# Kernel tuning notes

Hardware: AMD Instinct MI355X
Metric: run time of the kernel (lower is better)

Reference implementation:

```python
import jax, jax.numpy as jnp
import numpy as np
from jax import lax

ALPHA = 2.0       # spikingjelly ATan surrogate default alpha
NUM_HEADS = 8
V_TH = 1.0

@jax.custom_vjp
def spike(x):
    return (x >= 0.0).astype(x.dtype)

def _spike_fwd(x):
    return spike(x), x

def _spike_bwd(x, g):
    # ATan surrogate: alpha/2 / (1 + (pi/2 * alpha * x)^2)
    return (g * (ALPHA / 2.0) / (1.0 + (jnp.pi / 2.0 * ALPHA * x) ** 2),)

spike.defvjp(_spike_fwd, _spike_bwd)

def lif(x, w):
    # ParametricLIFNode, step_mode='m', decay_input=True, hard reset to 0,
    # detach_reset=True. x: [T, ...]; w: learned scalar, decay = sigmoid(w).
    decay = jax.nn.sigmoid(w)
    def step(v, xt):
        v = v + (xt - v) * decay
        s = spike(v - V_TH)
        v = v * (1.0 - lax.stop_gradient(s))  # detach_reset hard reset
        return v, s
    _, s = lax.scan(step, jnp.zeros_like(x[0]), x)
    return s

def layernorm(x, g, b, eps=1e-5):
    m = x.mean(-1, keepdims=True)
    var = ((x - m) ** 2).mean(-1, keepdims=True)
    return (x - m) / jnp.sqrt(var + eps) * g + b

def setup_inputs() -> dict:
    key = jax.random.key(0)
    ks = jax.random.split(key, 16)
    T, B, C, H, W = 4, 16, 512, 16, 16
    hidden = 4 * C
    s = 0.02
    inp = {
        'x': jax.random.normal(ks[0], (T, B, C, H, W), jnp.float32),
        'conv_w': jax.random.normal(ks[1], (C, 1, 3, 3), jnp.float32) * s,
        'conv_b': jnp.zeros((C,), jnp.float32),
        'ln1_g': jnp.ones((C,), jnp.float32),
        'ln1_b': jnp.zeros((C,), jnp.float32),
        'qkv_w': jax.random.normal(ks[2], (3 * C, C), jnp.float32) * s,
        'proj_w': jax.random.normal(ks[3], (C, C), jnp.float32) * s,
        'proj_b': jnp.zeros((C,), jnp.float32),
        'ln2_g': jnp.ones((C,), jnp.float32),
        'ln2_b': jnp.zeros((C,), jnp.float32),
        'fc1_w': jax.random.normal(ks[4], (hidden, C), jnp.float32) * s,
        'fc1_b': jnp.zeros((hidden,), jnp.float32),
        'fc2_w': jax.random.normal(ks[5], (C, hidden), jnp.float32) * s,
        'fc2_b': jnp.zeros((C,), jnp.float32),
        'lif_w': jnp.zeros((8,), jnp.float32),  # init_tau=2 -> w=0
    }
    return inp

def reference(x, conv_w, conv_b, ln1_g, ln1_b, qkv_w, proj_w, proj_b,
              ln2_g, ln2_b, fc1_w, fc1_b, fc2_w, fc2_b, lif_w):
    T, B, C, H, W = x.shape
    N = H * W
    nH = NUM_HEADS
    d = C // nH
    scale = d ** -0.5

    # conv positional embedding on spikes, residual
    s = lif(x, lif_w[0])
    sf = s.reshape(T * B, C, H, W)
    pos = lax.conv_general_dilated(
        sf, conv_w, (1, 1), 'SAME', feature_group_count=C,
        dimension_numbers=('NCHW', 'OIHW', 'NCHW'))
    pos = pos + conv_b[None, :, None, None]
    x = x + pos.reshape(T, B, C, H, W)

    # tokens: [T, B, N, C]
    xt = x.reshape(T, B, C, N).transpose(0, 1, 3, 2)

    # spiking linear attention
    h = lif(layernorm(xt, ln1_g, ln1_b), lif_w[1])
    qkv = h @ qkv_w.T                              # [T,B,N,3C]
    qkv = qkv.reshape(T, B, N, 3, nH, d).transpose(3, 0, 1, 4, 2, 5)  # [3,T,B,h,N,d]
    q = lif(qkv[0], lif_w[2])
    k = lif(qkv[1], lif_w[3])
    v = lif(qkv[2], lif_w[4])
    kv = jnp.einsum('tbhnd,tbhne->tbhde', k, v)    # [T,B,h,d,d]
    a = jnp.einsum('tbhnd,tbhde->tbhne', q, kv) * scale
    a = a.transpose(0, 1, 3, 2, 4).reshape(T, B, N, C)
    a = lif(a, lif_w[5])
    a = a @ proj_w.T + proj_b
    xt = xt + a

    # spiking MLP
    h = lif(layernorm(xt, ln2_g, ln2_b), lif_w[6])
    h = h @ fc1_w.T + fc1_b
    h = lif(h, lif_w[7])
    h = h @ fc2_w.T + fc2_b
    xt = xt + h

    return xt.transpose(0, 1, 3, 2).reshape(T, B, C, H, W)
```

## Files before the change

### kernel.cpp

```cpp
#include <hip/hip_runtime.h>

typedef unsigned long long u64;
typedef unsigned int u32;
typedef float  floatx4 __attribute__((ext_vector_type(4)));
typedef short  short8  __attribute__((ext_vector_type(8)));

#define T_ 4

static __device__ __forceinline__ float b2f(unsigned short u){
  union { unsigned int i; float f; } x; x.i = ((unsigned int)u) << 16; return x.f;
}
static __device__ __forceinline__ unsigned short f2b(float f){
  unsigned int u = __float_as_uint(f);
  unsigned int r = (u + 0x7FFFu + ((u >> 16) & 1u)) >> 16;
  return (unsigned short)r;
}
static __device__ __forceinline__ float sigmoidf_(float x){ return 1.f / (1.f + expf(-x)); }

static __device__ __forceinline__ void gll16(const void* g, void* l){
  __builtin_amdgcn_global_load_lds(
      (const __attribute__((address_space(1))) void*)g,
      (__attribute__((address_space(3))) void*)l, 16, 0, 0);
}

__global__ __launch_bounds__(256) void wsplit_kernel(const float* __restrict__ qkvw,
    const float* __restrict__ projw, const float* __restrict__ fc1w,
    const float* __restrict__ fc2w, unsigned short* __restrict__ hi,
    unsigned short* __restrict__ lo){
  int i = blockIdx.x * 256 + threadIdx.x;
  const float* src; int off;
  if (i < 786432)      { src = qkvw; off = i; }
  else if (i < 1048576){ src = projw; off = i - 786432; }
  else if (i < 2097152){ src = fc1w;  off = i - 1048576; }
  else                 { src = fc2w;  off = i - 2097152; }
  float f = src[off];
  unsigned short h = f2b(f);
  float r = f - b2f(h);
  hi[i] = h; lo[i] = f2b(r);
}

__global__ __launch_bounds__(256) void conv_lif_kernel(const float* __restrict__ x,
    const float* __restrict__ cw, const float* __restrict__ cb,
    const float* __restrict__ lifw, float* __restrict__ xt){
  __shared__ __align__(16) float xs[16 * 260];
  __shared__ u64 sbits[16][5];
  int bb = blockIdx.x & 15, cg = blockIdx.x >> 4;
  int c0 = cg * 16;
  int tid = threadIdx.x;
  int lane = tid & 63, w = tid >> 6;
  int cl = tid & 15;
  float D = sigmoidf_(lifw[0]);
  float cwv[9];
  #pragma unroll
  for (int j = 0; j < 9; ++j) cwv[j] = cw[(c0 + cl) * 9 + j];
  float cbv = cb[c0 + cl];
  float v[16];
  #pragma unroll
  for (int k = 0; k < 16; ++k) v[k] = 0.f;

  for (int t = 0; t < T_; ++t){
    #pragma unroll
    for (int j = 0; j < 4; ++j){
      int kk = __builtin_amdgcn_readfirstlane(w + 4 * j);
      const float* grow = x + (((size_t)t * 16 + bb) * 512 + c0 + kk) * 256 + lane * 4;
      gll16(grow, &xs[kk * 260]);
    }
    __syncthreads();
    #pragma unroll
    for (int k = 0; k < 16; ++k){
      float xv = xs[k * 260 + tid];
      v[k] = v[k] + (xv - v[k]) * D;
      bool sp = v[k] >= 1.f;
      u64 bal = __ballot(sp);
      if (lane == 0) sbits[k][w] = bal;
      v[k] = sp ? 0.f : v[k];
    }
    __syncthreads();
    u64 sw0 = sbits[cl][0], sw1 = sbits[cl][1], sw2 = sbits[cl][2], sw3 = sbits[cl][3];
    #pragma unroll
    for (int i = 0; i < 16; ++i){
      int n = (tid >> 4) + 16 * i;
      int hh = n >> 4, ww = n & 15;
      float acc = cbv;
      #pragma unroll
      for (int dy = -1; dy <= 1; ++dy){
        int yy = hh + dy; if ((unsigned)yy >= 16u) continue;
        #pragma unroll
        for (int dx = -1; dx <= 1; ++dx){
          int xx = ww + dx; if ((unsigned)xx >= 16u) continue;
          int p = yy * 16 + xx;
          u64 word = (p < 64) ? sw0 : (p < 128) ? sw1 : (p < 192) ? sw2 : sw3;
          if ((word >> (p & 63)) & 1ull) acc += cwv[(dy + 1) * 3 + (dx + 1)];
        }
      }
      float xv = xs[cl * 260 + n];
      xt[(((size_t)t * 16 + bb) * 256 + n) * 512 + c0 + cl] = xv + acc;
    }
    __syncthreads();
  }
}

__global__ __launch_bounds__(256) void ln_lif_kernel(const float* __restrict__ xt,
    const float* __restrict__ g, const float* __restrict__ be,
    const float* __restrict__ lifw, int lidx, u64* __restrict__ obits){
  int bn = blockIdx.x; int tid = threadIdx.x;
  int lane = tid & 63, wid = tid >> 6;
  int c0 = tid, c1 = tid + 256;
  __shared__ float ps[8];
  float D = sigmoidf_(lifw[lidx]);
  float g0 = g[c0], g1 = g[c1];
  float b0 = be[c0], b1 = be[c1];
  float v0 = 0.f, v1 = 0.f;
  for (int t = 0; t < T_; ++t){
    size_t base = ((size_t)t * 4096 + bn) * 512;
    float x0 = xt[base + c0], x1 = xt[base + c1];
    float s = x0 + x1, q = x0 * x0 + x1 * x1;
    #pragma unroll
    for (int m = 32; m > 0; m >>= 1){
      s += __shfl_xor(s, m, 64);
      q += __shfl_xor(q, m, 64);
    }
    if (lane == 0){ ps[wid * 2] = s; ps[wid * 2 + 1] = q; }
    __syncthreads();
    float S = ps[0] + ps[2] + ps[4] + ps[6];
    float Q = ps[1] + ps[3] + ps[5] + ps[7];
    __syncthreads();
    float mean = S * (1.f / 512.f);
    float var = Q * (1.f / 512.f) - mean * mean;
    float inv = 1.f / sqrtf(var + 1e-5f);
    float y0 = (x0 - mean) * inv * g0 + b0;
    float y1 = (x1 - mean) * inv * g1 + b1;
    v0 = v0 + (y0 - v0) * D; bool s0 = v0 >= 1.f;
    v1 = v1 + (y1 - v1) * D; bool s1 = v1 >= 1.f;
    u64 bal0 = __ballot(s0);
    u64 bal1 = __ballot(s1);
    if (lane == 0){
      size_t rb = ((size_t)t * 4096 + bn) * 8;
      obits[rb + wid] = bal0;
      obits[rb + 4 + wid] = bal1;
    }
    v0 = s0 ? 0.f : v0; v1 = s1 ? 0.f : v1;
  }
}

__global__ __launch_bounds__(256) void lif_bits_kernel(const float* __restrict__ in,
    u64* __restrict__ bits, const float* __restrict__ lifw, int lidx){
  int tid = blockIdx.x * 256 + threadIdx.x;
  int j = tid & 511; int bn = tid >> 9;
  float D = sigmoidf_(lifw[lidx]);
  float v = 0.f;
  #pragma unroll
  for (int t = 0; t < T_; ++t){
    int m = t * 4096 + bn;
    float xv = in[(size_t)m * 512 + j];
    v = v + (xv - v) * D;
    bool sp = v >= 1.f;
    u64 bal = __ballot(sp);
    if ((threadIdx.x & 63) == 0) bits[(size_t)m * 8 + (j >> 6)] = bal;
    v = sp ? 0.f : v;
  }
}

__global__ __launch_bounds__(256) void gemm_fused(
    const u64* __restrict__ Abits, int ars,
    const unsigned short* __restrict__ Whi, const unsigned short* __restrict__ Wlo, int ldw,
    const float* __restrict__ bias,
    float* __restrict__ xtio, float* __restrict__ outF,
    u64* __restrict__ outBits,
    int K, int mode, const float* __restrict__ lifw, int lidx){
  extern __shared__ __align__(16) char smemraw[];
  unsigned short* Bh = (unsigned short*)smemraw;
  unsigned short* Bl = (unsigned short*)(smemraw + 16384);
  u32* Alds = (u32*)(smemraw + 32768);
  u64* tab  = (u64*)(smemraw + 40960);
  int bn0 = blockIdx.x * 32;
  int n0  = blockIdx.y * 128;
  int tid = threadIdx.x, lane = tid & 63, wid = tid >> 6;
  int wn = wid * 32;
  int lm = lane & 15, quad = lane >> 4;
  int qs = quad * 8;
  int swz = ((lane & 3) ^ ((lane >> 3) & 3)) * 8;
  int rW = wn + (lane >> 2);
  const unsigned short* pH0 = Whi + (size_t)(n0 + rW) * ldw + swz;
  const unsigned short* pH1 = pH0 + (size_t)16 * ldw;
  const unsigned short* pL0 = Wlo + (size_t)(n0 + rW) * ldw + swz;
  const unsigned short* pL1 = pL0 + (size_t)16 * ldw;
  int b0 = __builtin_amdgcn_readfirstlane(wid << 10);
  int sx = (quad ^ ((lm >> 1) & 3)) << 3;

  auto stageA = [&](int w0){
    #pragma unroll
    for (int i = 0; i < 4; ++i){
      int idx = tid + i * 256;
      int r = idx & 127, w64 = idx >> 7;
      size_t g = (size_t)((r >> 5) * 4096 + bn0 + (r & 31));
      u64 vb = Abits[g * ars + w0 + w64];
      Alds[(2 * w64) * 128 + r]     = (u32)vb;
      Alds[(2 * w64 + 1) * 128 + r] = (u32)(vb >> 32);
    }
  };
  auto stageB = [&](int buf, int kb){
    int bo = (buf << 12) + b0;
    gll16(pH0 + kb, Bh + bo);
    gll16(pH1 + kb, Bh + bo + 512);
    gll16(pL0 + kb, Bl + bo);
    gll16(pL1 + kb, Bl + bo + 512);
  };

  if (tid < 16){
    u64 e = 0;
    #pragma unroll
    for (int j = 0; j < 4; ++j) if ((tid >> j) & 1) e |= 0x3F80ull << (16 * j);
    tab[tid] = e;
  }
  stageA(0);
  stageB(0, 0);
  stageB(1, 32);
  __syncthreads();

  floatx4 acc[8][2];
  #pragma unroll
  for (int i = 0; i < 8; ++i)
    #pragma unroll
    for (int j = 0; j < 2; ++j){ acc[i][j][0]=0.f; acc[i][j][1]=0.f; acc[i][j][2]=0.f; acc[i][j][3]=0.f; }

  int cur = 0;
  for (int kb = 0; kb < K; kb += 32){
    if (kb && (kb & 511) == 0){
      __syncthreads();
      stageA(kb >> 6);
      __syncthreads();
    }
    if (kb + 32 < K) asm volatile("s_waitcnt vmcnt(4)" ::: "memory");
    else             asm volatile("s_waitcnt vmcnt(0)" ::: "memory");
    __builtin_amdgcn_sched_barrier(0);
    int bo = cur << 12;
    int wl = (kb >> 5) & 15;
    short8 bh[2], bl[2];
    #pragma unroll
    for (int in = 0; in < 2; ++in){
      bh[in] = *(const short8*)(&Bh[bo + (wn + in * 16 + lm) * 32 + sx]);
      bl[in] = *(const short8*)(&Bl[bo + (wn + in * 16 + lm) * 32 + sx]);
    }
    __builtin_amdgcn_s_setprio(1);
    #pragma unroll
    for (int im = 0; im < 8; ++im){
      u32 wv = Alds[wl * 128 + im * 16 + lm];
      u32 by = wv >> qs;
      union { u64 d[2]; short8 s; } c;
      c.d[0] = tab[by & 15u];
      c.d[1] = tab[(by >> 4) & 15u];
      acc[im][0] = __builtin_amdgcn_mfma_f32_16x16x32_bf16(c.s, bh[0], acc[im][0], 0, 0, 0);
      acc[im][1] = __builtin_amdgcn_mfma_f32_16x16x32_bf16(c.s, bh[1], acc[im][1], 0, 0, 0);
      acc[im][0] = __builtin_amdgcn_mfma_f32_16x16x32_bf16(c.s, bl[0], acc[im][0], 0, 0, 0);
      acc[im][1] = __builtin_amdgcn_mfma_f32_16x16x32_bf16(c.s, bl[1], acc[im][1], 0, 0, 0);
    }
    __builtin_amdgcn_s_setprio(0);
    __builtin_amdgcn_sched_barrier(0);
    if (kb + 64 < K) stageB(cur, kb + 64);
    cur ^= 1;
  }

  if (mode == 0 || mode == 3){
    #pragma unroll
    for (int im = 0; im < 8; ++im){
      int row0 = im * 16 + quad * 4;
      #pragma unroll
      for (int in = 0; in < 2; ++in){
        int col = n0 + wn + in * 16 + lm;
        float bv = bias ? bias[col] : 0.f;
        #pragma unroll
        for (int r = 0; r < 4; ++r){
          int row = row0 + r;
          int t = row >> 5; int bq = bn0 + (row & 31);
          size_t gg = (size_t)t * 4096 + bq;
          float vv = acc[im][in][r] + bv + xtio[gg * 512 + col];
          if (mode == 0){
            xtio[gg * 512 + col] = vv;
          } else {
            outF[(((size_t)t * 16 + (bq >> 8)) * 512 + col) * 256 + (bq & 255)] = vv;
          }
        }
      }
    }
    return;
  }

  __syncthreads();
  u32* bits32 = (u32*)(smemraw + 32768);
  u64* ob; int obrs, obwb;
  if (mode == 1){ ob = outBits + (size_t)(n0 >> 9) * 131072; obrs = 8; obwb = (n0 & 511) >> 6; }
  else          { ob = outBits; obrs = 32; obwb = n0 >> 6; }
  float D = sigmoidf_(lifw[mode == 1 ? (2 + (n0 >> 9)) : lidx]);
  float bv0 = bias ? bias[n0 + wn + lm] : 0.f;
  float bv1 = bias ? bias[n0 + wn + 16 + lm] : 0.f;
  #pragma unroll
  for (int r = 0; r < 4; ++r){
    float vA0 = 0.f, vA1 = 0.f, vB0 = 0.f, vB1 = 0.f;
    #pragma unroll
    for (int t = 0; t < 4; ++t){
      float pA0 = acc[2*t][0][r] + bv0;   vA0 += (pA0 - vA0) * D; bool sA0 = vA0 >= 1.f; vA0 = sA0 ? 0.f : vA0;
      float pA1 = acc[2*t][1][r] + bv1;   vA1 += (pA1 - vA1) * D; bool sA1 = vA1 >= 1.f; vA1 = sA1 ? 0.f : vA1;
      float pB0 = acc[2*t+1][0][r] + bv0; vB0 += (pB0 - vB0) * D; bool sB0 = vB0 >= 1.f; vB0 = sB0 ? 0.f : vB0;
      float pB1 = acc[2*t+1][1][r] + bv1; vB1 += (pB1 - vB1) * D; bool sB1 = vB1 >= 1.f; vB1 = sB1 ? 0.f : vB1;
      u64 balA0 = __ballot(sA0), balA1 = __ballot(sA1);
      u64 balB0 = __ballot(sB0), balB1 = __ballot(sB1);
      if (lane < 4){
        int q = lane;
        u32 wA = (u32)((balA0 >> (16*q)) & 0xFFFFull) | ((u32)((balA1 >> (16*q)) & 0xFFFFull) << 16);
        u32 wB = (u32)((balB0 >> (16*q)) & 0xFFFFull) | ((u32)((balB1 >> (16*q)) & 0xFFFFull) << 16);
        bits32[(t * 32 + q * 4 + r) * 4 + wid]      = wA;
        bits32[(t * 32 + 16 + q * 4 + r) * 4 + wid] = wB;
      }
    }
  }
  __syncthreads();
  {
    int t = tid >> 6, bnl = (tid >> 1) & 31, j = tid & 1;
    size_t g = (size_t)t * 4096 + bn0 + bnl;
    int idx = (t * 32 + bnl) * 4 + 2 * j;
    u64 wv = (u64)bits32[idx] | ((u64)bits32[idx + 1] << 32);
    ob[g * obrs + obwb + j] = wv;
  }
}

__global__ __launch_bounds__(256) void attn_a_kernel(const u64* __restrict__ bits,
    float* __restrict__ aout){
  int tbh = blockIdx.x;
  int h = tbh & 7, b = (tbh >> 3) & 15, t = tbh >> 7;
  int m0 = t * 4096 + b * 256;
  int tid = threadIdx.x, lane = tid & 63, wid = tid >> 6;
  __shared__ u64 QW[256], KW[256], VW[256];
  __shared__ u64 kbt[64][4], vbt[64][4];
  __shared__ __align__(16) unsigned short Bs[64 * 72];
  {
    size_t base = (size_t)(m0 + tid) * 8 + h;
    QW[tid] = bits[base];
    KW[tid] = bits[131072 + base];
    VW[tid] = bits[262144 + base];
  }
  __syncthreads();
  {
    int i = tid & 63, w = tid >> 6;
    const u64* kwp = &KW[w * 64];
    const u64* vwp = &VW[w * 64];
    u64 bk = 0, bv = 0;
    for (int nn = 0; nn < 64; ++nn){
      bk |= ((kwp[nn] >> i) & 1ull) << nn;
      bv |= ((vwp[nn] >> i) & 1ull) << nn;
    }
    kbt[i][w] = bk; vbt[i][w] = bv;
  }
  __syncthreads();
  #pragma unroll
  for (int e = 0; e < 16; ++e){
    int idx = tid * 16 + e;
    int i = idx >> 6, j = idx & 63;
    int cnt = __popcll(kbt[i][0] & vbt[j][0]) + __popcll(kbt[i][1] & vbt[j][1])
            + __popcll(kbt[i][2] & vbt[j][2]) + __popcll(kbt[i][3] & vbt[j][3]);
    Bs[j * 72 + i] = f2b((float)cnt);
  }
  __syncthreads();
  int lm = lane & 15, quad = lane >> 4;
  int wm = wid * 64;
  u64 qw[4];
  #pragma unroll
  for (int im = 0; im < 4; ++im) qw[im] = QW[wm + im * 16 + lm];
  floatx4 acc[4][4];
  #pragma unroll
  for (int i = 0; i < 4; ++i)
    #pragma unroll
    for (int j = 0; j < 4; ++j){ acc[i][j][0]=0.f; acc[i][j][1]=0.f; acc[i][j][2]=0.f; acc[i][j][3]=0.f; }
  #pragma unroll
  for (int kb = 0; kb < 64; kb += 32){
    short8 af[4], bf[4];
    #pragma unroll
    for (int im = 0; im < 4; ++im){
      u32 byte = (u32)(qw[im] >> (kb + quad * 8)) & 0xFFu;
      union { u32 u[4]; short8 s; } c;
      c.u[0] = ((byte & 1u)        | ((byte & 2u) << 15))        * 0x3F80u;
      c.u[1] = (((byte >> 2) & 1u) | (((byte >> 3) & 1u) << 16)) * 0x3F80u;
      c.u[2] = (((byte >> 4) & 1u) | (((byte >> 5) & 1u) << 16)) * 0x3F80u;
      c.u[3] = (((byte >> 6) & 1u) | (((byte >> 7) & 1u) << 16)) * 0x3F80u;
      af[im] = c.s;
    }
    #pragma unroll
    for (int in = 0; in < 4; ++in)
      bf[in] = *(const short8*)(&Bs[(in * 16 + lm) * 72 + kb + quad * 8]);
    #pragma unroll
    for (int im = 0; im < 4; ++im)
      #pragma unroll
      for (int in = 0; in < 4; ++in)
        acc[im][in] = __builtin_amdgcn_mfma_f32_16x16x32_bf16(af[im], bf[in], acc[im][in], 0, 0, 0);
  }
  float* ob = aout + (size_t)m0 * 512 + h * 64;
  #pragma unroll
  for (int im = 0; im < 4; ++im){
    int nr0 = wm + im * 16 + quad * 4;
    #pragma unroll
    for (int in = 0; in < 4; ++in){
      int j = in * 16 + lm;
      #pragma unroll
      for (int r = 0; r < 4; ++r)
        ob[(size_t)(nr0 + r) * 512 + j] = acc[im][in][r] * 0.125f;
    }
  }
}

extern "C" void kernel_launch(void* const* d_in, const int* in_sizes, int n_in,
                              void* d_out, int out_size, void* d_ws, size_t ws_size,
                              hipStream_t stream){
  const float* x     = (const float*)d_in[0];
  const float* convw = (const float*)d_in[1];
  const float* convb = (const float*)d_in[2];
  const float* ln1g  = (const float*)d_in[3];
  const float* ln1b  = (const float*)d_in[4];
  const float* qkvw  = (const float*)d_in[5];
  const float* projw = (const float*)d_in[6];
  const float* projb = (const float*)d_in[7];
  const float* ln2g  = (const float*)d_in[8];
  const float* ln2b  = (const float*)d_in[9];
  const float* fc1w  = (const float*)d_in[10];
  const float* fc1b  = (const float*)d_in[11];
  const float* fc2w  = (const float*)d_in[12];
  const float* fc2b  = (const float*)d_in[13];
  const float* lifw  = (const float*)d_in[14];
  float* outp = (float*)d_out;

  char* wsb = (char*)d_ws;
  float* XT           = (float*)wsb;
  float* AF32         = (float*)(wsb + 33554432);
  unsigned short* WHI = (unsigned short*)(wsb + 67108864);
  unsigned short* WLO = (unsigned short*)(wsb + 73400320);
  u64* QBITS          = (u64*)(wsb + 79691776);
  u64* H12            = (u64*)(wsb + 82837504);
  u64* ASB            = (u64*)(wsb + 83886080);
  u64* HBITS          = (u64*)(wsb + 84934656);
  const int OFF_QKV = 0, OFF_PROJ = 786432, OFF_FC1 = 1048576, OFF_FC2 = 2097152;
  const int GEMM_LDS = 41088;

  wsplit_kernel<<<12288, 256, 0, stream>>>(qkvw, projw, fc1w, fc2w, WHI, WLO);
  conv_lif_kernel<<<512, 256, 0, stream>>>(x, convw, convb, lifw, XT);
  ln_lif_kernel<<<4096, 256, 0, stream>>>(XT, ln1g, ln1b, lifw, 1, H12);
  gemm_fused<<<dim3(128, 12), 256, GEMM_LDS, stream>>>(H12, 8,
      WHI + OFF_QKV, WLO + OFF_QKV, 512, nullptr,
      nullptr, nullptr, QBITS, 512, 1, lifw, 0);
  attn_a_kernel<<<512, 256, 0, stream>>>(QBITS, AF32);
  lif_bits_kernel<<<8192, 256, 0, stream>>>(AF32, ASB, lifw, 5);
  gemm_fused<<<dim3(128, 4), 256, GEMM_LDS, stream>>>(ASB, 8,
      WHI + OFF_PROJ, WLO + OFF_PROJ, 512, projb,
      XT, nullptr, nullptr, 512, 0, lifw, 0);
  ln_lif_kernel<<<4096, 256, 0, stream>>>(XT, ln2g, ln2b, lifw, 6, H12);
  gemm_fused<<<dim3(128, 16), 256, GEMM_LDS, stream>>>(H12, 8,
      WHI + OFF_FC1, WLO + OFF_FC1, 512, fc1b,
      nullptr, nullptr, HBITS, 512, 2, lifw, 7);
  gemm_fused<<<dim3(128, 4), 256, GEMM_LDS, stream>>>(HBITS, 32,
      WHI + OFF_FC2, WLO + OFF_FC2, 2048, fc2b,
      XT, outp, nullptr, 2048, 3, lifw, 0);
}
```

Baseline: 396.8 us.

## Switch fused spike GEMM from 16x16x32 to 32x32x16 MFMA tiles

Replaces the 16x16x32 bf16 MFMA with the 32x32x16 variant in the bit-packed spike GEMM. Each wave now holds four 32x32 accumulators, one per timestep, instead of eight 16x16 pairs. The B-fragment reads, the A-bit unpacking, the residual epilogue and the LIF ballot epilogue are all remapped to the 32x32 output layout. The aim is fewer MFMA issues per unit of work and cheaper operand and A-table loads, at the cost of a new swizzle and index mapping that must be exactly right.

```diff
diff --git a/kernel.cpp b/kernel.cpp
--- a/kernel.cpp
+++ b/kernel.cpp
@@ -2,8 +2,9 @@
 
 typedef unsigned long long u64;
 typedef unsigned int u32;
-typedef float  floatx4 __attribute__((ext_vector_type(4)));
-typedef short  short8  __attribute__((ext_vector_type(8)));
+typedef float  floatx4  __attribute__((ext_vector_type(4)));
+typedef float  floatx16 __attribute__((ext_vector_type(16)));
+typedef short  short8   __attribute__((ext_vector_type(8)));
 
 #define T_ 4
 
@@ -177,8 +178,9 @@
   int n0  = blockIdx.y * 128;
   int tid = threadIdx.x, lane = tid & 63, wid = tid >> 6;
   int wn = wid * 32;
-  int lm = lane & 15, quad = lane >> 4;
-  int qs = quad * 8;
+  int nl = lane & 31;
+  int kh = lane >> 5;
+  int fN = (nl >> 1) & 3;
   int swz = ((lane & 3) ^ ((lane >> 3) & 3)) * 8;
   int rW = wn + (lane >> 2);
   const unsigned short* pH0 = Whi + (size_t)(n0 + rW) * ldw + swz;
@@ -186,7 +188,6 @@
   const unsigned short* pL0 = Wlo + (size_t)(n0 + rW) * ldw + swz;
   const unsigned short* pL1 = pL0 + (size_t)16 * ldw;
   int b0 = __builtin_amdgcn_readfirstlane(wid << 10);
-  int sx = (quad ^ ((lm >> 1) & 3)) << 3;
 
   auto stageA = [&](int w0){
     #pragma unroll
@@ -218,11 +219,11 @@
   stageB(1, 32);
   __syncthreads();
 
-  floatx4 acc[8][2];
-  #pragma unroll
-  for (int i = 0; i < 8; ++i)
-    #pragma unroll
-    for (int j = 0; j < 2; ++j){ acc[i][j][0]=0.f; acc[i][j][1]=0.f; acc[i][j][2]=0.f; acc[i][j][3]=0.f; }
+  floatx16 acc[4];
+  #pragma unroll
+  for (int i = 0; i < 4; ++i)
+    #pragma unroll
+    for (int e = 0; e < 16; ++e) acc[i][e] = 0.f;
 
   int cur = 0;
   for (int kb = 0; kb < K; kb += 32){
@@ -238,22 +239,26 @@
     int wl = (kb >> 5) & 15;
     short8 bh[2], bl[2];
     #pragma unroll
-    for (int in = 0; in < 2; ++in){
-      bh[in] = *(const short8*)(&Bh[bo + (wn + in * 16 + lm) * 32 + sx]);
-      bl[in] = *(const short8*)(&Bl[bo + (wn + in * 16 + lm) * 32 + sx]);
-    }
+    for (int h = 0; h < 2; ++h){
+      int slot = (((2 * h + kh) ^ fN) << 3);
+      bh[h] = *(const short8*)(&Bh[bo + (wn + nl) * 32 + slot]);
+      bl[h] = *(const short8*)(&Bl[bo + (wn + nl) * 32 + slot]);
+    }
+    u32 wv[4];
+    #pragma unroll
+    for (int mb = 0; mb < 4; ++mb) wv[mb] = Alds[wl * 128 + mb * 32 + nl];
     __builtin_amdgcn_s_setprio(1);
     #pragma unroll
-    for (int im = 0; im < 8; ++im){
-      u32 wv = Alds[wl * 128 + im * 16 + lm];
-      u32 by = wv >> qs;
-      union { u64 d[2]; short8 s; } c;
-      c.d[0] = tab[by & 15u];
-      c.d[1] = tab[(by >> 4) & 15u];
-      acc[im][0] = __builtin_amdgcn_mfma_f32_16x16x32_bf16(c.s, bh[0], acc[im][0], 0, 0, 0);
-      acc[im][1] = __builtin_amdgcn_mfma_f32_16x16x32_bf16(c.s, bh[1], acc[im][1], 0, 0, 0);
-      acc[im][0] = __builtin_amdgcn_mfma_f32_16x16x32_bf16(c.s, bl[0], acc[im][0], 0, 0, 0);
-      acc[im][1] = __builtin_amdgcn_mfma_f32_16x16x32_bf16(c.s, bl[1], acc[im][1], 0, 0, 0);
+    for (int mb = 0; mb < 4; ++mb){
+      #pragma unroll
+      for (int h = 0; h < 2; ++h){
+        u32 by = (wv[mb] >> (16 * h + 8 * kh)) & 0xFFu;
+        union { u64 d[2]; short8 s; } c;
+        c.d[0] = tab[by & 15u];
+        c.d[1] = tab[(by >> 4) & 15u];
+        acc[mb] = __builtin_amdgcn_mfma_f32_32x32x16_bf16(c.s, bh[h], acc[mb], 0, 0, 0);
+        acc[mb] = __builtin_amdgcn_mfma_f32_32x32x16_bf16(c.s, bl[h], acc[mb], 0, 0, 0);
+      }
     }
     __builtin_amdgcn_s_setprio(0);
     __builtin_amdgcn_sched_barrier(0);
@@ -262,24 +267,20 @@
   }
 
   if (mode == 0 || mode == 3){
-    #pragma unroll
-    for (int im = 0; im < 8; ++im){
-      int row0 = im * 16 + quad * 4;
+    int col = n0 + wn + nl;
+    float bv = bias ? bias[col] : 0.f;
+    #pragma unroll
+    for (int mb = 0; mb < 4; ++mb){
       #pragma unroll
-      for (int in = 0; in < 2; ++in){
-        int col = n0 + wn + in * 16 + lm;
-        float bv = bias ? bias[col] : 0.f;
-        #pragma unroll
-        for (int r = 0; r < 4; ++r){
-          int row = row0 + r;
-          int t = row >> 5; int bq = bn0 + (row & 31);
-          size_t gg = (size_t)t * 4096 + bq;
-          float vv = acc[im][in][r] + bv + xtio[gg * 512 + col];
-          if (mode == 0){
-            xtio[gg * 512 + col] = vv;
-          } else {
-            outF[(((size_t)t * 16 + (bq >> 8)) * 512 + col) * 256 + (bq & 255)] = vv;
-          }
+      for (int reg = 0; reg < 16; ++reg){
+        int tok = (reg & 3) + 8 * (reg >> 2) + 4 * kh;
+        int bq = bn0 + tok;
+        size_t gg = (size_t)mb * 4096 + bq;
+        float vv = acc[mb][reg] + bv + xtio[gg * 512 + col];
+        if (mode == 0){
+          xtio[gg * 512 + col] = vv;
+        } else {
+          outF[(((size_t)mb * 16 + (bq >> 8)) * 512 + col) * 256 + (bq & 255)] = vv;
         }
       }
     }
@@ -292,25 +293,20 @@
   if (mode == 1){ ob = outBits + (size_t)(n0 >> 9) * 131072; obrs = 8; obwb = (n0 & 511) >> 6; }
   else          { ob = outBits; obrs = 32; obwb = n0 >> 6; }
   float D = sigmoidf_(lifw[mode == 1 ? (2 + (n0 >> 9)) : lidx]);
-  float bv0 = bias ? bias[n0 + wn + lm] : 0.f;
-  float bv1 = bias ? bias[n0 + wn + 16 + lm] : 0.f;
-  #pragma unroll
-  for (int r = 0; r < 4; ++r){
-    float vA0 = 0.f, vA1 = 0.f, vB0 = 0.f, vB1 = 0.f;
+  int col = n0 + wn + nl;
+  float bv = bias ? bias[col] : 0.f;
+  #pragma unroll
+  for (int reg = 0; reg < 16; ++reg){
+    int tokL = (reg & 3) + 8 * (reg >> 2);
+    float v = 0.f;
     #pragma unroll
     for (int t = 0; t < 4; ++t){
-      float pA0 = acc[2*t][0][r] + bv0;   vA0 += (pA0 - vA0) * D; bool sA0 = vA0 >= 1.f; vA0 = sA0 ? 0.f : vA0;
-      float pA1 = acc[2*t][1][r] + bv1;   vA1 += (pA1 - vA1) * D; bool sA1 = vA1 >= 1.f; vA1 = sA1 ? 0.f : vA1;
-      float pB0 = acc[2*t+1][0][r] + bv0; vB0 += (pB0 - vB0) * D; bool sB0 = vB0 >= 1.f; vB0 = sB0 ? 0.f : vB0;
-      float pB1 = acc[2*t+1][1][r] + bv1; vB1 += (pB1 - vB1) * D; bool sB1 = vB1 >= 1.f; vB1 = sB1 ? 0.f : vB1;
-      u64 balA0 = __ballot(sA0), balA1 = __ballot(sA1);
-      u64 balB0 = __ballot(sB0), balB1 = __ballot(sB1);
-      if (lane < 4){
-        int q = lane;
-        u32 wA = (u32)((balA0 >> (16*q)) & 0xFFFFull) | ((u32)((balA1 >> (16*q)) & 0xFFFFull) << 16);
-        u32 wB = (u32)((balB0 >> (16*q)) & 0xFFFFull) | ((u32)((balB1 >> (16*q)) & 0xFFFFull) << 16);
-        bits32[(t * 32 + q * 4 + r) * 4 + wid]      = wA;
-        bits32[(t * 32 + 16 + q * 4 + r) * 4 + wid] = wB;
+      float p = acc[t][reg] + bv;
+      v += (p - v) * D; bool sp = v >= 1.f; v = sp ? 0.f : v;
+      u64 bal = __ballot(sp);
+      if (lane == 0){
+        bits32[(t * 32 + tokL) * 4 + wid]     = (u32)bal;
+        bits32[(t * 32 + tokL + 4) * 4 + wid] = (u32)(bal >> 32);
       }
     }
   }
```

Result: slower. 424.9 us (+7.1%).

## Split K across two warp groups in proj and fc2 GEMMs with LDS reduction

Applied to the files above, without the earlier changes.

Templates the fused GEMM on a group count. The proj and fc2 launches now use 512-thread blocks whose two 4-wave groups each handle half of K, then reduce through LDS before the residual epilogue. The A-bit staging is reorganised to 256-wide K chunks per group, and the GROUPS=1 LDS size shrinks. The intent is more waves in flight for the narrow N=512 GEMMs, which only launch 512 blocks; the cost is doubled LDS per block and an extra LDS reduction with barriers.

```diff
diff --git a/kernel.cpp b/kernel.cpp
--- a/kernel.cpp
+++ b/kernel.cpp
@@ -161,46 +161,55 @@
   }
 }
 
-__global__ __launch_bounds__(256) void gemm_fused(
+template<int GROUPS>
+__global__ __launch_bounds__(GROUPS * 256, 4) void gemm_fused(
     const u64* __restrict__ Abits, int ars,
     const unsigned short* __restrict__ Whi, const unsigned short* __restrict__ Wlo, int ldw,
     const float* __restrict__ bias,
     float* __restrict__ xtio, float* __restrict__ outF,
     u64* __restrict__ outBits,
     int K, int mode, const float* __restrict__ lifw, int lidx){
+  constexpr int NT = GROUPS * 256;
   extern __shared__ __align__(16) char smemraw[];
   unsigned short* Bh = (unsigned short*)smemraw;
-  unsigned short* Bl = (unsigned short*)(smemraw + 16384);
-  u32* Alds = (u32*)(smemraw + 32768);
-  u64* tab  = (u64*)(smemraw + 40960);
+  unsigned short* Bl = (unsigned short*)(smemraw + GROUPS * 16384);
+  u32* Alds = (u32*)(smemraw + GROUPS * 32768);
+  u64* tab  = (u64*)(smemraw + GROUPS * 32768 + GROUPS * 4096);
+  const int KH = K / GROUPS;
   int bn0 = blockIdx.x * 32;
   int n0  = blockIdx.y * 128;
   int tid = threadIdx.x, lane = tid & 63, wid = tid >> 6;
-  int wn = wid * 32;
+  int grp = (GROUPS == 2) ? (wid >> 2) : 0;
+  int wv  = wid & 3;
+  int wn = wv * 32;
   int lm = lane & 15, quad = lane >> 4;
   int qs = quad * 8;
   int swz = ((lane & 3) ^ ((lane >> 3) & 3)) * 8;
+  int kbase = grp * KH;
   int rW = wn + (lane >> 2);
-  const unsigned short* pH0 = Whi + (size_t)(n0 + rW) * ldw + swz;
+  const unsigned short* pH0 = Whi + (size_t)(n0 + rW) * ldw + swz + kbase;
   const unsigned short* pH1 = pH0 + (size_t)16 * ldw;
-  const unsigned short* pL0 = Wlo + (size_t)(n0 + rW) * ldw + swz;
+  const unsigned short* pL0 = Wlo + (size_t)(n0 + rW) * ldw + swz + kbase;
   const unsigned short* pL1 = pL0 + (size_t)16 * ldw;
-  int b0 = __builtin_amdgcn_readfirstlane(wid << 10);
+  int gb  = __builtin_amdgcn_readfirstlane(grp * 8192);
+  int wb  = __builtin_amdgcn_readfirstlane(grp * 8192 + wv * 1024);
   int sx = (quad ^ ((lm >> 1) & 3)) << 3;
 
-  auto stageA = [&](int w0){
-    #pragma unroll
-    for (int i = 0; i < 4; ++i){
-      int idx = tid + i * 256;
-      int r = idx & 127, w64 = idx >> 7;
-      size_t g = (size_t)((r >> 5) * 4096 + bn0 + (r & 31));
-      u64 vb = Abits[g * ars + w0 + w64];
-      Alds[(2 * w64) * 128 + r]     = (u32)vb;
-      Alds[(2 * w64 + 1) * 128 + r] = (u32)(vb >> 32);
+  auto stageA = [&](int c){
+    #pragma unroll
+    for (int i = 0; i < 2; ++i){
+      int idx = tid + i * NT;
+      int r = idx & 127;
+      int q = idx >> 7;
+      int g = q >> 2, w = q & 3;
+      size_t grow = (size_t)((r >> 5) * 4096 + bn0 + (r & 31));
+      u64 vb = Abits[grow * ars + (size_t)g * (KH >> 6) + c * 4 + w];
+      Alds[g * 1024 + (2 * w) * 128 + r]     = (u32)vb;
+      Alds[g * 1024 + (2 * w + 1) * 128 + r] = (u32)(vb >> 32);
     }
   };
   auto stageB = [&](int buf, int kb){
-    int bo = (buf << 12) + b0;
+    int bo = wb + (buf << 12);
     gll16(pH0 + kb, Bh + bo);
     gll16(pH1 + kb, Bh + bo + 512);
     gll16(pL0 + kb, Bl + bo);
@@ -225,17 +234,17 @@
     for (int j = 0; j < 2; ++j){ acc[i][j][0]=0.f; acc[i][j][1]=0.f; acc[i][j][2]=0.f; acc[i][j][3]=0.f; }
 
   int cur = 0;
-  for (int kb = 0; kb < K; kb += 32){
-    if (kb && (kb & 511) == 0){
+  for (int kb = 0; kb < KH; kb += 32){
+    if (kb && (kb & 255) == 0){
       __syncthreads();
-      stageA(kb >> 6);
+      stageA(kb >> 8);
       __syncthreads();
     }
-    if (kb + 32 < K) asm volatile("s_waitcnt vmcnt(4)" ::: "memory");
-    else             asm volatile("s_waitcnt vmcnt(0)" ::: "memory");
+    if (kb + 32 < KH) asm volatile("s_waitcnt vmcnt(4)" ::: "memory");
+    else              asm volatile("s_waitcnt vmcnt(0)" ::: "memory");
     __builtin_amdgcn_sched_barrier(0);
-    int bo = cur << 12;
-    int wl = (kb >> 5) & 15;
+    int bo = gb + (cur << 12);
+    int wl = (kb >> 5) & 7;
     short8 bh[2], bl[2];
     #pragma unroll
     for (int in = 0; in < 2; ++in){
@@ -245,8 +254,8 @@
     __builtin_amdgcn_s_setprio(1);
     #pragma unroll
     for (int im = 0; im < 8; ++im){
-      u32 wv = Alds[wl * 128 + im * 16 + lm];
-      u32 by = wv >> qs;
+      u32 wv32 = Alds[grp * 1024 + wl * 128 + im * 16 + lm];
+      u32 by = wv32 >> qs;
       union { u64 d[2]; short8 s; } c;
       c.d[0] = tab[by & 15u];
       c.d[1] = tab[(by >> 4) & 15u];
@@ -257,11 +266,30 @@
     }
     __builtin_amdgcn_s_setprio(0);
     __builtin_amdgcn_sched_barrier(0);
-    if (kb + 64 < K) stageB(cur, kb + 64);
+    if (kb + 64 < KH) stageB(cur, kb + 64);
     cur ^= 1;
   }
 
   if (mode == 0 || mode == 3){
+    float* X = (float*)smemraw;
+    if constexpr (GROUPS == 2){
+      __syncthreads();
+      if (grp == 1){
+        #pragma unroll
+        for (int im = 0; im < 8; ++im){
+          int row0 = im * 16 + quad * 4;
+          #pragma unroll
+          for (int in = 0; in < 2; ++in){
+            int cl_ = wn + in * 16 + lm;
+            #pragma unroll
+            for (int r = 0; r < 4; ++r)
+              X[(row0 + r) * 132 + cl_] = acc[im][in][r];
+          }
+        }
+      }
+      __syncthreads();
+      if (grp == 1) return;
+    }
     #pragma unroll
     for (int im = 0; im < 8; ++im){
       int row0 = im * 16 + quad * 4;
@@ -275,6 +303,7 @@
           int t = row >> 5; int bq = bn0 + (row & 31);
           size_t gg = (size_t)t * 4096 + bq;
           float vv = acc[im][in][r] + bv + xtio[gg * 512 + col];
+          if constexpr (GROUPS == 2) vv += X[row * 132 + wn + in * 16 + lm];
           if (mode == 0){
             xtio[gg * 512 + col] = vv;
           } else {
@@ -286,41 +315,43 @@
     return;
   }
 
-  __syncthreads();
-  u32* bits32 = (u32*)(smemraw + 32768);
-  u64* ob; int obrs, obwb;
-  if (mode == 1){ ob = outBits + (size_t)(n0 >> 9) * 131072; obrs = 8; obwb = (n0 & 511) >> 6; }
-  else          { ob = outBits; obrs = 32; obwb = n0 >> 6; }
-  float D = sigmoidf_(lifw[mode == 1 ? (2 + (n0 >> 9)) : lidx]);
-  float bv0 = bias ? bias[n0 + wn + lm] : 0.f;
-  float bv1 = bias ? bias[n0 + wn + 16 + lm] : 0.f;
-  #pragma unroll
-  for (int r = 0; r < 4; ++r){
-    float vA0 = 0.f, vA1 = 0.f, vB0 = 0.f, vB1 = 0.f;
-    #pragma unroll
-    for (int t = 0; t < 4; ++t){
-      float pA0 = acc[2*t][0][r] + bv0;   vA0 += (pA0 - vA0) * D; bool sA0 = vA0 >= 1.f; vA0 = sA0 ? 0.f : vA0;
-      float pA1 = acc[2*t][1][r] + bv1;   vA1 += (pA1 - vA1) * D; bool sA1 = vA1 >= 1.f; vA1 = sA1 ? 0.f : vA1;
-      float pB0 = acc[2*t+1][0][r] + bv0; vB0 += (pB0 - vB0) * D; bool sB0 = vB0 >= 1.f; vB0 = sB0 ? 0.f : vB0;
-      float pB1 = acc[2*t+1][1][r] + bv1; vB1 += (pB1 - vB1) * D; bool sB1 = vB1 >= 1.f; vB1 = sB1 ? 0.f : vB1;
-      u64 balA0 = __ballot(sA0), balA1 = __ballot(sA1);
-      u64 balB0 = __ballot(sB0), balB1 = __ballot(sB1);
-      if (lane < 4){
-        int q = lane;
-        u32 wA = (u32)((balA0 >> (16*q)) & 0xFFFFull) | ((u32)((balA1 >> (16*q)) & 0xFFFFull) << 16);
-        u32 wB = (u32)((balB0 >> (16*q)) & 0xFFFFull) | ((u32)((balB1 >> (16*q)) & 0xFFFFull) << 16);
-        bits32[(t * 32 + q * 4 + r) * 4 + wid]      = wA;
-        bits32[(t * 32 + 16 + q * 4 + r) * 4 + wid] = wB;
+  if constexpr (GROUPS == 1){
+    __syncthreads();
+    u32* bits32 = (u32*)(smemraw + 32768);
+    u64* ob; int obrs, obwb;
+    if (mode == 1){ ob = outBits + (size_t)(n0 >> 9) * 131072; obrs = 8; obwb = (n0 & 511) >> 6; }
+    else          { ob = outBits; obrs = 32; obwb = n0 >> 6; }
+    float D = sigmoidf_(lifw[mode == 1 ? (2 + (n0 >> 9)) : lidx]);
+    float bv0 = bias ? bias[n0 + wn + lm] : 0.f;
+    float bv1 = bias ? bias[n0 + wn + 16 + lm] : 0.f;
+    #pragma unroll
+    for (int r = 0; r < 4; ++r){
+      float vA0 = 0.f, vA1 = 0.f, vB0 = 0.f, vB1 = 0.f;
+      #pragma unroll
+      for (int t = 0; t < 4; ++t){
+        float pA0 = acc[2*t][0][r] + bv0;   vA0 += (pA0 - vA0) * D; bool sA0 = vA0 >= 1.f; vA0 = sA0 ? 0.f : vA0;
+        float pA1 = acc[2*t][1][r] + bv1;   vA1 += (pA1 - vA1) * D; bool sA1 = vA1 >= 1.f; vA1 = sA1 ? 0.f : vA1;
+        float pB0 = acc[2*t+1][0][r] + bv0; vB0 += (pB0 - vB0) * D; bool sB0 = vB0 >= 1.f; vB0 = sB0 ? 0.f : vB0;
+        float pB1 = acc[2*t+1][1][r] + bv1; vB1 += (pB1 - vB1) * D; bool sB1 = vB1 >= 1.f; vB1 = sB1 ? 0.f : vB1;
+        u64 balA0 = __ballot(sA0), balA1 = __ballot(sA1);
+        u64 balB0 = __ballot(sB0), balB1 = __ballot(sB1);
+        if (lane < 4){
+          int q = lane;
+          u32 wA = (u32)((balA0 >> (16*q)) & 0xFFFFull) | ((u32)((balA1 >> (16*q)) & 0xFFFFull) << 16);
+          u32 wB = (u32)((balB0 >> (16*q)) & 0xFFFFull) | ((u32)((balB1 >> (16*q)) & 0xFFFFull) << 16);
+          bits32[(t * 32 + q * 4 + r) * 4 + wid]      = wA;
+          bits32[(t * 32 + 16 + q * 4 + r) * 4 + wid] = wB;
+        }
       }
     }
-  }
-  __syncthreads();
-  {
-    int t = tid >> 6, bnl = (tid >> 1) & 31, j = tid & 1;
-    size_t g = (size_t)t * 4096 + bn0 + bnl;
-    int idx = (t * 32 + bnl) * 4 + 2 * j;
-    u64 wv = (u64)bits32[idx] | ((u64)bits32[idx + 1] << 32);
-    ob[g * obrs + obwb + j] = wv;
+    __syncthreads();
+    {
+      int t = tid >> 6, bnl = (tid >> 1) & 31, j = tid & 1;
+      size_t g = (size_t)t * 4096 + bn0 + bnl;
+      int idx = (t * 32 + bnl) * 4 + 2 * j;
+      u64 wv64 = (u64)bits32[idx] | ((u64)bits32[idx + 1] << 32);
+      ob[g * obrs + obwb + j] = wv64;
+    }
   }
 }
 
@@ -437,24 +468,25 @@
   u64* ASB            = (u64*)(wsb + 83886080);
   u64* HBITS          = (u64*)(wsb + 84934656);
   const int OFF_QKV = 0, OFF_PROJ = 786432, OFF_FC1 = 1048576, OFF_FC2 = 2097152;
-  const int GEMM_LDS = 41088;
+  const int LDS1 = 36992;
+  const int LDS2 = 73856;
 
   wsplit_kernel<<<12288, 256, 0, stream>>>(qkvw, projw, fc1w, fc2w, WHI, WLO);
   conv_lif_kernel<<<512, 256, 0, stream>>>(x, convw, convb, lifw, XT);
   ln_lif_kernel<<<4096, 256, 0, stream>>>(XT, ln1g, ln1b, lifw, 1, H12);
-  gemm_fused<<<dim3(128, 12), 256, GEMM_LDS, stream>>>(H12, 8,
+  gemm_fused<1><<<dim3(128, 12), 256, LDS1, stream>>>(H12, 8,
       WHI + OFF_QKV, WLO + OFF_QKV, 512, nullptr,
       nullptr, nullptr, QBITS, 512, 1, lifw, 0);
   attn_a_kernel<<<512, 256, 0, stream>>>(QBITS, AF32);
   lif_bits_kernel<<<8192, 256, 0, stream>>>(AF32, ASB, lifw, 5);
-  gemm_fused<<<dim3(128, 4), 256, GEMM_LDS, stream>>>(ASB, 8,
+  gemm_fused<2><<<dim3(128, 4), 512, LDS2, stream>>>(ASB, 8,
       WHI + OFF_PROJ, WLO + OFF_PROJ, 512, projb,
       XT, nullptr, nullptr, 512, 0, lifw, 0);
   ln_lif_kernel<<<4096, 256, 0, stream>>>(XT, ln2g, ln2b, lifw, 6, H12);
-  gemm_fused<<<dim3(128, 16), 256, GEMM_LDS, stream>>>(H12, 8,
+  gemm_fused<1><<<dim3(128, 16), 256, LDS1, stream>>>(H12, 8,
       WHI + OFF_FC1, WLO + OFF_FC1, 512, fc1b,
       nullptr, nullptr, HBITS, 512, 2, lifw, 7);
-  gemm_fused<<<dim3(128, 4), 256, GEMM_LDS, stream>>>(HBITS, 32,
+  gemm_fused<2><<<dim3(128, 4), 512, LDS2, stream>>>(HBITS, 32,
       WHI + OFF_FC2, WLO + OFF_FC2, 2048, fc2b,
       XT, outp, nullptr, 2048, 3, lifw, 0);
 }
```

After: 375.8 us. 1.06x faster.
